# Kernel optimization log

Hardware: AMD Instinct MI355X
Metric: run time of the kernel (lower is better)

The kernel has to match this reference:

```python
import jax, jax.numpy as jnp
import numpy as np

PERIOD = 24
NUM_ITERATIONS = 2


def _window_size():
    w = max(3, PERIOD // 2)  # 12
    if w % 2 == 0:
        w += 1  # 13
    return w


def moving_average(s, w):
    # s: [N, L]; replicate-pad by w//2 on each side, then width-w mean conv ('VALID')
    pad = w // 2
    sp = jnp.pad(s, ((0, 0), (pad, pad)), mode='edge')[:, None, :]  # [N,1,L+2*pad]
    k = jnp.ones((1, 1, w), s.dtype) / w
    y = jax.lax.conv_general_dilated(sp, k, window_strides=(1,), padding='VALID',
                                     dimension_numbers=('NCH', 'OIH', 'NCH'))
    return y[:, 0, :]  # [N, L]


def extract_seasonal(d):
    # d: [N, L] with L a multiple of PERIOD. Strided indices i, i+P, ... correspond
    # to reshape [N, C, P] with fixed last axis; median over cycles, broadcast back.
    N, L = d.shape
    C = L // PERIOD
    sub = d.reshape(N, C, PERIOD)
    med = jnp.median(sub, axis=1)  # [N, P] (C=121 is odd -> matches torch.median)
    return jnp.broadcast_to(med[:, None, :], (N, C, PERIOD)).reshape(N, L)


def setup_inputs() -> dict:
    key = jax.random.key(0)
    x = jax.random.normal(key, (64, 2904, 207), dtype=jnp.float32)
    return {"x": x}


def reference(x):
    # x: [B, L, F] -> process all features at once as [B*F, L]
    B, L, F = x.shape
    s = jnp.transpose(x, (0, 2, 1)).reshape(B * F, L)
    w = _window_size()
    trend = moving_average(s, w)
    for _ in range(NUM_ITERATIONS):
        seasonal = extract_seasonal(s - trend)
        trend = moving_average(s - seasonal, w)
    residual = s - trend - seasonal

    def unflatten(a):
        return jnp.transpose(a.reshape(B, F, L), (0, 2, 1))  # [B, L, F]

    return unflatten(trend), unflatten(seasonal), unflatten(residual)
```

## Files before the change

kernel.cpp:

```cpp
#include <hip/hip_runtime.h>

#define LROW    2904
#define PERIOD  24
#define CYC     121
#define NF      207
#define KF      208
#define NB      64
#define NROWS   13248
#define NSLOT   61
#define NT      256
#define LTILE   24
#define NLT     121
#define K2GRID  (NB * NLT)
#define K2CHUNK (K2GRID / 8)
#define R13     (1.f / 13.f)

typedef unsigned short us2 __attribute__((ext_vector_type(2)));

__device__ __forceinline__ int clampi(int i) {
    return i < 0 ? 0 : (i >= LROW ? LROW - 1 : i);
}
__device__ __forceinline__ unsigned quantk(float d) {
    int ki = (int)fmaf(d, 4096.f, 32768.f);
    ki = ki < 0 ? 0 : (ki > 65535 ? 65535 : ki);
    return (unsigned)ki;
}
__device__ __forceinline__ float dqmid(unsigned k) {
    return ((float)(int)k - 32767.5f) * (1.f / 4096.f);
}

__device__ __forceinline__ unsigned selN_split(const unsigned (&K)[31], int thr) {
    unsigned T = 0;
    const us2 one2 = __builtin_bit_cast(us2, 0x00010001u);
    for (int bit = 15; bit >= 0; --bit) {
        unsigned Tp = T | (1u << bit);
        unsigned tm32 = (Tp - 1u) | ((Tp - 1u) << 16);
        us2 tm2 = __builtin_bit_cast(us2, tm32);
        us2 acc = __builtin_bit_cast(us2, 0u);
        #pragma unroll
        for (int s = 0; s < 31; ++s) {
            us2 kv = __builtin_bit_cast(us2, K[s]);
            us2 dd = __builtin_elementwise_sub_sat(kv, tm2);
            us2 mm = __builtin_elementwise_min(dd, one2);
            acc = acc + mm;
        }
        unsigned a = __builtin_bit_cast(unsigned, acc);
        int cnt = (int)(a & 0xFFFFu) + (int)(a >> 16);
        cnt += __shfl_xor(cnt, 1);
        if (cnt >= thr) T = Tp;
    }
    return T;
}

__global__ __launch_bounds__(256) void k_keys(const float* __restrict__ x,
                                              unsigned* __restrict__ keys) {
    __shared__ float T[62 * NF];
    const int b  = blockIdx.x;
    const int cp = blockIdx.y;
    const int fl = threadIdx.x;
    const int fe = fl < NF ? fl : NF - 1;
    const int l0 = cp * 48;
    const float* xb = x + (size_t)b * (LROW * NF);
    unsigned* kb = keys + ((size_t)b * PERIOD * NSLOT + cp) * KF + fl;

    if (cp != 0 && cp != 60) {
        const float2* s2 = (const float2*)(xb + (size_t)(l0 - 8) * NF);
        float2* t2 = (float2*)T;
        for (int i = fl; i < 62 * NF / 2; i += NT) t2[i] = s2[i];
    } else {
        for (int i = fl; i < 62 * NF; i += NT) {
            int lr = i / NF, ff = i - lr * NF;
            T[i] = xb[(size_t)clampi(l0 - 8 + lr) * NF + ff];
        }
    }
    __syncthreads();

    float r[13];
    #pragma unroll
    for (int i = 0; i < 13; ++i) r[i] = T[(i + 1) * NF + fe];
    float sum = ((r[0]+r[1])+(r[2]+r[3]))+((r[4]+r[5])+(r[6]+r[7]))
              + ((r[8]+r[9])+(r[10]+r[11])) + r[12];

    if (cp < 60) {
        unsigned pend[PERIOD];
        #pragma unroll
        for (int j = 0; j < 48; ++j) {
            float xn = T[(j + 14) * NF + fe];
            sum += xn - r[0];
            unsigned k = quantk(r[7] - sum * R13);
            if (j < 24) pend[j] = k;
            else if (fl < KF)
                __builtin_nontemporal_store(pend[j - 24] | (k << 16),
                                            &kb[(size_t)(j - 24) * (NSLOT * KF)]);
            #pragma unroll
            for (int i = 0; i < 12; ++i) r[i] = r[i + 1];
            r[12] = xn;
        }
    } else {
        #pragma unroll
        for (int j = 0; j < 24; ++j) {
            float xn = T[(j + 14) * NF + fe];
            sum += xn - r[0];
            unsigned k = quantk(r[7] - sum * R13);
            if (fl < KF)
                __builtin_nontemporal_store(k | 0xFFFF0000u,
                                            &kb[(size_t)j * (NSLOT * KF)]);
            #pragma unroll
            for (int i = 0; i < 12; ++i) r[i] = r[i + 1];
            r[12] = xn;
        }
    }
}

__global__ __launch_bounds__(256) void k_med0(const unsigned* __restrict__ keys,
                                              unsigned short* __restrict__ m0key) {
    const int d  = blockIdx.x;
    const int bp = (d & 7) * 192 + (d >> 3);
    const int fb = blockIdx.y;
    const int t  = threadIdx.x;
    const int f  = fb * 128 + (t >> 1);
    const int half = t & 1;
    const int fx = f < KF ? f : KF - 1;

    const unsigned* kp = keys + (size_t)bp * (NSLOT * KF) + fx
                       + (half ? (size_t)30 * KF : 0);
    unsigned K[31];
    #pragma unroll
    for (int s = 0; s < 31; ++s) K[s] = kp[(size_t)s * KF];
    if (!half) K[30] = 0;

    unsigned T = selN_split(K, 62);
    if (!half && f < KF) m0key[(size_t)bp * KF + f] = (unsigned short)T;
}

__global__ __launch_bounds__(256) void k_edge2(const unsigned* __restrict__ keys,
                                               const unsigned short* __restrict__ m0key,
                                               float* __restrict__ medBedge) {
    const int d  = blockIdx.x;
    const int be = (d & 7) * 96 + (d >> 3);
    const int b = be / 12, e = be - 12 * b;
    const int p = (e < 6) ? e : e + 12;
    const int fb = blockIdx.y;
    const int t  = threadIdx.x;
    const int f  = fb * 128 + (t >> 1);
    const int half = t & 1;
    const int fx = f < KF ? f : KF - 1;

    float m0[PERIOD];
    #pragma unroll
    for (int q = 0; q < PERIOD; ++q)
        m0[q] = dqmid(m0key[(size_t)(b * PERIOD + q) * KF + fx]);

    float wph = 0.f, we = 0.f;
    #pragma unroll
    for (int ee = 0; ee < 12; ++ee) if (ee == e) {
        const int pp = (ee < 6) ? ee : ee + 12;
        #pragma unroll
        for (int q = 0; q < 13; ++q) wph += m0[(pp + 18 + q) % 24];
        #pragma unroll
        for (int q = -6; q <= 6; ++q) {
            int aa = pp + q; if (aa < 0) aa = 0; if (aa > 23) aa = 23;
            we += m0[aa];
        }
    }

    const unsigned* kp = keys + (size_t)(b * PERIOD + p) * (NSLOT * KF) + fx
                       + (half ? (size_t)30 * KF : 0);
    unsigned K[31];
    #pragma unroll
    for (int s = 0; s < 31; ++s) K[s] = kp[(size_t)s * KF];
    if (!half) K[30] = 0;

    unsigned m = (unsigned)m0key[(size_t)(b * PERIOD + p) * KF + fx];
    unsigned xk = keys[(size_t)(b * PERIOD + p) * (NSLOT * KF)
                       + (size_t)(p < 6 ? 0 : 60) * KF + fx] & 0xFFFFu;
    unsigned y = quantk(dqmid(xk) + (we - wph) * R13);

    int thr = (y > m) ? 61 : 63;
    unsigned v = selN_split(K, thr);
    bool up = (y > m) && (xk <= m);
    bool dn = (y < m) && (xk >= m);
    unsigned nm = up ? (y < v ? y : v) : (dn ? (y > v ? y : v) : m);
    if (!half && f < KF)
        medBedge[(size_t)(b * 12 + e) * KF + f] = dqmid(nm) + wph * R13;
}

__global__ __launch_bounds__(NT, 5) void stl_outputs(const float* __restrict__ x,
                                                     const unsigned short* __restrict__ m0key,
                                                     const float* __restrict__ medBedge,
                                                     float* __restrict__ out) {
    __shared__ float T[(LTILE + 12) * NF];

    const int d   = blockIdx.x;
    const int blk = (d & 7) * K2CHUNK + (d >> 3);
    const int b  = blk / NLT;
    const int kk = blk - b * NLT;
    const int l0 = kk * LTILE;
    const int t  = threadIdx.x;
    const float* xb = x + (size_t)b * (LROW * NF);

    if (kk != 0 && kk != NLT - 1) {
        const float2* s2 = (const float2*)(xb + (size_t)(l0 - 6) * NF);
        float2* t2 = (float2*)T;
        for (int i = t; i < (LTILE + 12) * NF / 2; i += NT) t2[i] = s2[i];
    } else {
        for (int i = t; i < (LTILE + 12) * NF; i += NT) {
            int lr = i / NF;
            int ff = i - lr * NF;
            T[i] = xb[(size_t)clampi(l0 - 6 + lr) * NF + ff];
        }
    }
    __syncthreads();

    if (t < NF) {
        float m0[PERIOD];
        #pragma unroll
        for (int q = 0; q < PERIOD; ++q)
            m0[q] = dqmid(m0key[(size_t)(b * PERIOD + q) * KF + t]);
        float W0[PERIOD];
        {
            float s = 0.f;
            #pragma unroll
            for (int q = 0; q < 13; ++q) s += m0[q];
            W0[0] = s;
            #pragma unroll
            for (int q = 1; q < PERIOD; ++q)
                W0[q] = W0[q - 1] + m0[(q + 12) % 24] - m0[q - 1];
        }
        float lm[PERIOD];
        #pragma unroll
        for (int e = 0; e < 12; ++e) {
            int p = (e < 6) ? e : e + 12;
            lm[p] = medBedge[(size_t)(b * 12 + e) * KF + t];
        }
        #pragma unroll
        for (int p = 6; p < 18; ++p) lm[p] = m0[p] + W0[p - 6] * R13;
        float wt[PERIOD];
        {
            float s = 0.f;
            #pragma unroll
            for (int q = 0; q < 13; ++q) s += lm[q];
            wt[0] = s;
            #pragma unroll
            for (int q = 1; q < PERIOD; ++q)
                wt[q] = wt[q - 1] + lm[(q + 12) % 24] - lm[q - 1];
        }

        float s13 = 0.f;
        #pragma unroll
        for (int r = 0; r < 13; ++r) s13 += T[r * NF + t];

        const bool edgeLo = (kk == 0), edgeHi = (kk == NLT - 1);
        const size_t S = (size_t)NROWS * LROW;
        const size_t obase = (size_t)b * (LROW * NF) + (size_t)l0 * NF + (size_t)t;

        #pragma unroll
        for (int j = 0; j < LTILE; ++j) {
            float W = wt[(j + 18) % 24];
            if (edgeLo && j < 6) {
                float w = 0.f;
                #pragma unroll
                for (int jj = -6; jj <= 6; ++jj) { int m = j + jj; if (m < 0) m = 0; w += lm[m]; }
                W = w;
            }
            if (edgeHi && j >= 18) {
                float w = 0.f;
                #pragma unroll
                for (int jj = -6; jj <= 6; ++jj) { int m = j + jj; if (m > 23) m = 23; w += lm[m]; }
                W = w;
            }
            float tr = (s13 - W) * R13;
            float se = lm[j];
            float re = T[(j + 6) * NF + t] - tr - se;
            size_t o = obase + (size_t)(j * NF);
            __builtin_nontemporal_store(tr, &out[o]);
            __builtin_nontemporal_store(se, &out[S + o]);
            __builtin_nontemporal_store(re, &out[2 * S + o]);
            if (j < LTILE - 1)
                s13 += T[(j + 13) * NF + t] - T[j * NF + t];
        }
    }
}

extern "C" void kernel_launch(void* const* d_in, const int* in_sizes, int n_in,
                              void* d_out, int out_size, void* d_ws, size_t ws_size,
                              hipStream_t stream) {
    const float* x = (const float*)d_in[0];
    float* out = (float*)d_out;
    float* wsf = (float*)d_ws;
    (void)in_sizes; (void)n_in; (void)out_size; (void)ws_size;

    unsigned*       keys     = (unsigned*)wsf;
    unsigned short* m0key    = (unsigned short*)(wsf + 19489792);
    float*          medBedge = wsf + 19489792 + 159744;

    hipLaunchKernelGGL(k_keys,   dim3(NB, NSLOT), dim3(NT), 0, stream, x, keys);
    hipLaunchKernelGGL(k_med0,   dim3(NB * PERIOD, 2), dim3(NT), 0, stream, keys, m0key);
    hipLaunchKernelGGL(k_edge2,  dim3(NB * 12, 2), dim3(NT), 0, stream, keys, m0key, medBedge);
    hipLaunchKernelGGL(stl_outputs, dim3(K2GRID), dim3(NT), 0, stream,
                       x, m0key, medBedge, out);
}
```

Measured before the change: 335.2 us.

## Fuse key generation and median selection into one LDS-resident kernel

Merges the key-building, initial-median and edge-median kernels into a single kernel. Each block handles one batch and an 8-feature chunk, builds the quantized keys directly into LDS, and runs both selection passes there, so the roughly 78MB keys buffer is never written to or read back from global memory. The per-feature lm/wt tables are also computed once per batch and stored, instead of being recomputed in every output block. In exchange, global reads of x are strided per feature (8 features per row segment), which coalesces poorly. Each block also needs a large LDS allocation, which may limit occupancy.

```diff
diff --git a/kernel.cpp b/kernel.cpp
--- a/kernel.cpp
+++ b/kernel.cpp
@@ -4,10 +4,12 @@
 #define PERIOD  24
 #define CYC     121
 #define NF      207
-#define KF      208
 #define NB      64
 #define NROWS   13248
-#define NSLOT   61
+#define FCH     8
+#define NCH     26
+#define KPADW   9
+#define KLDS    (PERIOD * 61 * KPADW)
 #define NT      256
 #define LTILE   24
 #define NLT     121
@@ -52,142 +54,171 @@
     return T;
 }
 
-__global__ __launch_bounds__(256) void k_keys(const float* __restrict__ x,
-                                              unsigned* __restrict__ keys) {
-    __shared__ float T[62 * NF];
-    const int b  = blockIdx.x;
-    const int cp = blockIdx.y;
-    const int fl = threadIdx.x;
-    const int fe = fl < NF ? fl : NF - 1;
-    const int l0 = cp * 48;
-    const float* xb = x + (size_t)b * (LROW * NF);
-    unsigned* kb = keys + ((size_t)b * PERIOD * NSLOT + cp) * KF + fl;
-
-    if (cp != 0 && cp != 60) {
-        const float2* s2 = (const float2*)(xb + (size_t)(l0 - 8) * NF);
-        float2* t2 = (float2*)T;
-        for (int i = fl; i < 62 * NF / 2; i += NT) t2[i] = s2[i];
+__device__ __forceinline__ void loadK31(const unsigned* keyl, int p, int f,
+                                        int half, unsigned (&K)[31]) {
+    const int base = p * 61 * KPADW + f;
+    if (!half) {
+        #pragma unroll
+        for (int s = 0; s < 31; ++s) K[s] = keyl[base + s * KPADW];
     } else {
-        for (int i = fl; i < 62 * NF; i += NT) {
-            int lr = i / NF, ff = i - lr * NF;
-            T[i] = xb[(size_t)clampi(l0 - 8 + lr) * NF + ff];
-        }
-    }
-    __syncthreads();
-
-    float r[13];
-    #pragma unroll
-    for (int i = 0; i < 13; ++i) r[i] = T[(i + 1) * NF + fe];
-    float sum = ((r[0]+r[1])+(r[2]+r[3]))+((r[4]+r[5])+(r[6]+r[7]))
-              + ((r[8]+r[9])+(r[10]+r[11])) + r[12];
-
-    if (cp < 60) {
-        unsigned pend[PERIOD];
-        #pragma unroll
-        for (int j = 0; j < 48; ++j) {
-            float xn = T[(j + 14) * NF + fe];
+        #pragma unroll
+        for (int s = 0; s < 30; ++s) K[s] = keyl[base + (31 + s) * KPADW];
+        K[30] = 0u;
+    }
+}
+
+__global__ __launch_bounds__(256) void k_median(const float* __restrict__ x,
+                                                float* __restrict__ wsTab) {
+    __shared__ unsigned keyl[KLDS];
+    __shared__ unsigned short m0s[PERIOD * FCH];
+    __shared__ float medBs[12 * FCH];
+
+    const int d   = blockIdx.x;
+    const int blk = (d & 7) * 208 + (d >> 3);
+    const int b   = blk & 63;
+    const int ch  = blk >> 6;
+    const int f0  = ch * FCH;
+    const int t   = threadIdx.x;
+
+    for (int i = t; i < KLDS; i += NT) keyl[i] = 0xFFFFFFFFu;
+    __syncthreads();
+
+    {
+        const int f   = t & 7;
+        const int seg = t >> 3;
+        const int fe  = (f0 + f < NF) ? (f0 + f) : (NF - 1);
+        const float* xb = x + (size_t)b * (LROW * NF) + fe;
+        const int l0 = seg * 91;
+        int c = l0 / PERIOD;
+        int p = l0 - c * PERIOD;
+        unsigned short* k16 = (unsigned short*)keyl;
+
+        float r[13];
+        float sum = 0.f;
+        #pragma unroll
+        for (int i = 0; i < 13; ++i) {
+            int li = l0 - 7 + i; if (li < 0) li = 0;
+            r[i] = xb[(size_t)li * NF];
+            sum += r[i];
+        }
+        #pragma unroll 13
+        for (int j = 0; j < 91; ++j) {
+            const int l = l0 + j;
+            int la = l + 6; if (la > LROW - 1) la = LROW - 1;
+            float xn = xb[(size_t)la * NF];
             sum += xn - r[0];
             unsigned k = quantk(r[7] - sum * R13);
-            if (j < 24) pend[j] = k;
-            else if (fl < KF)
-                __builtin_nontemporal_store(pend[j - 24] | (k << 16),
-                                            &kb[(size_t)(j - 24) * (NSLOT * KF)]);
+            if (l < LROW) {
+                int idx = (p * 61 + (c >> 1)) * KPADW + f;
+                k16[idx * 2 + (c & 1)] = (unsigned short)k;
+            }
             #pragma unroll
             for (int i = 0; i < 12; ++i) r[i] = r[i + 1];
             r[12] = xn;
-        }
-    } else {
-        #pragma unroll
-        for (int j = 0; j < 24; ++j) {
-            float xn = T[(j + 14) * NF + fe];
-            sum += xn - r[0];
-            unsigned k = quantk(r[7] - sum * R13);
-            if (fl < KF)
-                __builtin_nontemporal_store(k | 0xFFFF0000u,
-                                            &kb[(size_t)j * (NSLOT * KF)]);
-            #pragma unroll
-            for (int i = 0; i < 12; ++i) r[i] = r[i + 1];
-            r[12] = xn;
-        }
-    }
-}
-
-__global__ __launch_bounds__(256) void k_med0(const unsigned* __restrict__ keys,
-                                              unsigned short* __restrict__ m0key) {
-    const int d  = blockIdx.x;
-    const int bp = (d & 7) * 192 + (d >> 3);
-    const int fb = blockIdx.y;
-    const int t  = threadIdx.x;
-    const int f  = fb * 128 + (t >> 1);
-    const int half = t & 1;
-    const int fx = f < KF ? f : KF - 1;
-
-    const unsigned* kp = keys + (size_t)bp * (NSLOT * KF) + fx
-                       + (half ? (size_t)30 * KF : 0);
-    unsigned K[31];
-    #pragma unroll
-    for (int s = 0; s < 31; ++s) K[s] = kp[(size_t)s * KF];
-    if (!half) K[30] = 0;
-
-    unsigned T = selN_split(K, 62);
-    if (!half && f < KF) m0key[(size_t)bp * KF + f] = (unsigned short)T;
-}
-
-__global__ __launch_bounds__(256) void k_edge2(const unsigned* __restrict__ keys,
-                                               const unsigned short* __restrict__ m0key,
-                                               float* __restrict__ medBedge) {
-    const int d  = blockIdx.x;
-    const int be = (d & 7) * 96 + (d >> 3);
-    const int b = be / 12, e = be - 12 * b;
-    const int p = (e < 6) ? e : e + 12;
-    const int fb = blockIdx.y;
-    const int t  = threadIdx.x;
-    const int f  = fb * 128 + (t >> 1);
-    const int half = t & 1;
-    const int fx = f < KF ? f : KF - 1;
-
-    float m0[PERIOD];
-    #pragma unroll
-    for (int q = 0; q < PERIOD; ++q)
-        m0[q] = dqmid(m0key[(size_t)(b * PERIOD + q) * KF + fx]);
-
-    float wph = 0.f, we = 0.f;
-    #pragma unroll
-    for (int ee = 0; ee < 12; ++ee) if (ee == e) {
-        const int pp = (ee < 6) ? ee : ee + 12;
-        #pragma unroll
-        for (int q = 0; q < 13; ++q) wph += m0[(pp + 18 + q) % 24];
-        #pragma unroll
-        for (int q = -6; q <= 6; ++q) {
-            int aa = pp + q; if (aa < 0) aa = 0; if (aa > 23) aa = 23;
-            we += m0[aa];
-        }
-    }
-
-    const unsigned* kp = keys + (size_t)(b * PERIOD + p) * (NSLOT * KF) + fx
-                       + (half ? (size_t)30 * KF : 0);
-    unsigned K[31];
-    #pragma unroll
-    for (int s = 0; s < 31; ++s) K[s] = kp[(size_t)s * KF];
-    if (!half) K[30] = 0;
-
-    unsigned m = (unsigned)m0key[(size_t)(b * PERIOD + p) * KF + fx];
-    unsigned xk = keys[(size_t)(b * PERIOD + p) * (NSLOT * KF)
-                       + (size_t)(p < 6 ? 0 : 60) * KF + fx] & 0xFFFFu;
-    unsigned y = quantk(dqmid(xk) + (we - wph) * R13);
-
-    int thr = (y > m) ? 61 : 63;
-    unsigned v = selN_split(K, thr);
-    bool up = (y > m) && (xk <= m);
-    bool dn = (y < m) && (xk >= m);
-    unsigned nm = up ? (y < v ? y : v) : (dn ? (y > v ? y : v) : m);
-    if (!half && f < KF)
-        medBedge[(size_t)(b * 12 + e) * KF + f] = dqmid(nm) + wph * R13;
+            ++p; if (p == PERIOD) { p = 0; ++c; }
+        }
+    }
+    __syncthreads();
+
+    {
+        const int sel = t >> 1, half = t & 1;
+        const int f = sel & 7, p = sel >> 3;
+        unsigned K[31]; loadK31(keyl, p, f, half, K);
+        unsigned T = selN_split(K, 62);
+        if (!half) m0s[p * FCH + f] = (unsigned short)T;
+    }
+    if (t < 128) {
+        const int sel = t >> 1, half = t & 1;
+        const int f = sel & 7, p = 16 + (sel >> 3);
+        unsigned K[31]; loadK31(keyl, p, f, half, K);
+        unsigned T = selN_split(K, 62);
+        if (!half) m0s[p * FCH + f] = (unsigned short)T;
+    }
+    __syncthreads();
+
+    if (t < 192) {
+        const int sel = t >> 1, half = t & 1;
+        const int f = sel & 7, e = sel >> 3;
+        const int p = (e < 6) ? e : e + 12;
+
+        float m0[PERIOD];
+        #pragma unroll
+        for (int q = 0; q < PERIOD; ++q)
+            m0[q] = dqmid(m0s[q * FCH + f]);
+
+        float wph = 0.f, we = 0.f;
+        #pragma unroll
+        for (int ee = 0; ee < 12; ++ee) if (ee == e) {
+            const int pp = (ee < 6) ? ee : ee + 12;
+            #pragma unroll
+            for (int q = 0; q < 13; ++q) wph += m0[(pp + 18 + q) % 24];
+            #pragma unroll
+            for (int q = -6; q <= 6; ++q) {
+                int aa = pp + q; if (aa < 0) aa = 0; if (aa > 23) aa = 23;
+                we += m0[aa];
+            }
+        }
+
+        unsigned K[31]; loadK31(keyl, p, f, half, K);
+        unsigned m = (unsigned)m0s[p * FCH + f];
+        unsigned xk = ((unsigned short*)keyl)
+                      [((p * 61 + (p < 6 ? 0 : 60)) * KPADW + f) * 2];
+        unsigned y = quantk(dqmid(xk) + (we - wph) * R13);
+
+        int thr = (y > m) ? 61 : 63;
+        unsigned v = selN_split(K, thr);
+        bool up = (y > m) && (xk <= m);
+        bool dn = (y < m) && (xk >= m);
+        unsigned nm = up ? (y < v ? y : v) : (dn ? (y > v ? y : v) : m);
+        if (!half) medBs[e * FCH + f] = dqmid(nm) + wph * R13;
+    }
+    __syncthreads();
+
+    if (t < FCH && f0 + t < NF) {
+        const int f = t;
+        float m0[PERIOD];
+        #pragma unroll
+        for (int q = 0; q < PERIOD; ++q)
+            m0[q] = dqmid(m0s[q * FCH + f]);
+        float W0[PERIOD];
+        {
+            float s = 0.f;
+            #pragma unroll
+            for (int q = 0; q < 13; ++q) s += m0[q];
+            W0[0] = s;
+            #pragma unroll
+            for (int q = 1; q < PERIOD; ++q)
+                W0[q] = W0[q - 1] + m0[(q + 12) % 24] - m0[q - 1];
+        }
+        float lm[PERIOD];
+        #pragma unroll
+        for (int e = 0; e < 12; ++e) {
+            int p = (e < 6) ? e : e + 12;
+            lm[p] = medBs[e * FCH + f];
+        }
+        #pragma unroll
+        for (int p = 6; p < 18; ++p) lm[p] = m0[p] + W0[p - 6] * R13;
+        float wt[PERIOD];
+        {
+            float s = 0.f;
+            #pragma unroll
+            for (int q = 0; q < 13; ++q) s += lm[q];
+            wt[0] = s;
+            #pragma unroll
+            for (int q = 1; q < PERIOD; ++q)
+                wt[q] = wt[q - 1] + lm[(q + 12) % 24] - lm[q - 1];
+        }
+        float* wrow = wsTab + (size_t)b * 48 * NF + (f0 + f);
+        #pragma unroll
+        for (int i = 0; i < PERIOD; ++i) {
+            wrow[(size_t)i * NF]        = lm[i];
+            wrow[(size_t)(24 + i) * NF] = wt[i];
+        }
+    }
 }
 
 __global__ __launch_bounds__(NT, 5) void stl_outputs(const float* __restrict__ x,
-                                                     const unsigned short* __restrict__ m0key,
-                                                     const float* __restrict__ medBedge,
+                                                     const float* __restrict__ ws,
                                                      float* __restrict__ out) {
     __shared__ float T[(LTILE + 12) * NF];
 
@@ -213,38 +244,12 @@
     __syncthreads();
 
     if (t < NF) {
-        float m0[PERIOD];
-        #pragma unroll
-        for (int q = 0; q < PERIOD; ++q)
-            m0[q] = dqmid(m0key[(size_t)(b * PERIOD + q) * KF + t]);
-        float W0[PERIOD];
-        {
-            float s = 0.f;
-            #pragma unroll
-            for (int q = 0; q < 13; ++q) s += m0[q];
-            W0[0] = s;
-            #pragma unroll
-            for (int q = 1; q < PERIOD; ++q)
-                W0[q] = W0[q - 1] + m0[(q + 12) % 24] - m0[q - 1];
-        }
-        float lm[PERIOD];
-        #pragma unroll
-        for (int e = 0; e < 12; ++e) {
-            int p = (e < 6) ? e : e + 12;
-            lm[p] = medBedge[(size_t)(b * 12 + e) * KF + t];
-        }
-        #pragma unroll
-        for (int p = 6; p < 18; ++p) lm[p] = m0[p] + W0[p - 6] * R13;
-        float wt[PERIOD];
-        {
-            float s = 0.f;
-            #pragma unroll
-            for (int q = 0; q < 13; ++q) s += lm[q];
-            wt[0] = s;
-            #pragma unroll
-            for (int q = 1; q < PERIOD; ++q)
-                wt[q] = wt[q - 1] + lm[(q + 12) % 24] - lm[q - 1];
-        }
+        float lm[PERIOD], wt[PERIOD];
+        const float* wrow = ws + (size_t)b * 48 * NF + t;
+        #pragma unroll
+        for (int i = 0; i < PERIOD; ++i) lm[i] = wrow[(size_t)i * NF];
+        #pragma unroll
+        for (int i = 0; i < PERIOD; ++i) wt[i] = wrow[(size_t)(PERIOD + i) * NF];
 
         float s13 = 0.f;
         #pragma unroll
@@ -287,16 +292,10 @@
                               hipStream_t stream) {
     const float* x = (const float*)d_in[0];
     float* out = (float*)d_out;
-    float* wsf = (float*)d_ws;
+    float* wsTab = (float*)d_ws;
     (void)in_sizes; (void)n_in; (void)out_size; (void)ws_size;
 
-    unsigned*       keys     = (unsigned*)wsf;
-    unsigned short* m0key    = (unsigned short*)(wsf + 19489792);
-    float*          medBedge = wsf + 19489792 + 159744;
-
-    hipLaunchKernelGGL(k_keys,   dim3(NB, NSLOT), dim3(NT), 0, stream, x, keys);
-    hipLaunchKernelGGL(k_med0,   dim3(NB * PERIOD, 2), dim3(NT), 0, stream, keys, m0key);
-    hipLaunchKernelGGL(k_edge2,  dim3(NB * 12, 2), dim3(NT), 0, stream, keys, m0key, medBedge);
+    hipLaunchKernelGGL(k_median, dim3(NB * NCH), dim3(NT), 0, stream, x, wsTab);
     hipLaunchKernelGGL(stl_outputs, dim3(K2GRID), dim3(NT), 0, stream,
-                       x, m0key, medBedge, out);
-}
+                       x, wsTab, out);
+}
```

Result: slower. 406.6 us (+21.3%).
